# Optimization experiments

Measured on AMD Instinct MI355X. Metric: run time of the kernel, lower is better.

## Reference

```python
import jax, jax.numpy as jnp
import numpy as np
import math

B, N, H, D = 2, 2048, 16, 64

def setup_inputs() -> dict:
    key = jax.random.key(0)
    kq, kk, kv = jax.random.split(key, 3)
    q = jax.random.normal(kq, (B, N, H, D), dtype=jnp.float32)
    k = jax.random.normal(kk, (B, N, H, D), dtype=jnp.float32)
    v = jax.random.normal(kv, (B, N, H, D), dtype=jnp.float32)
    return {"q": q, "k": k, "v": v}

def reference(q, k, v):
    d = q.shape[-1]
    # [b,n,h,d] -> [b,h,n,d]
    qh = jnp.transpose(q, (0, 2, 1, 3))
    kh = jnp.transpose(k, (0, 2, 1, 3))
    vh = jnp.transpose(v, (0, 2, 1, 3))
    # scores: [b,h,n,n]
    scores = jnp.einsum('bhqd,bhkd->bhqk', qh, kh) / math.sqrt(d)
    # jax.nn.softmax performs the stable max-subtraction internally,
    # matching the original's explicit max-subtract + softmax.
    attn = jax.nn.softmax(scores, axis=-1)
    o = jnp.einsum('bhqk,bhkd->bhqd', attn, vh)
    # back to [b,n,h,d]
    return jnp.transpose(o, (0, 2, 1, 3))
```

## Files before the change

### kernel.cpp

```cpp
#include <hip/hip_runtime.h>


typedef float  f32x4  __attribute__((ext_vector_type(4)));
typedef float  f32x16 __attribute__((ext_vector_type(16)));
typedef short  s16x8  __attribute__((ext_vector_type(8)));
typedef short  s16x4  __attribute__((ext_vector_type(4)));
typedef int    i32x4  __attribute__((ext_vector_type(4)));

#define QSCALE 0.18033688011112042f

__device__ __forceinline__ unsigned short bf16r(float f) {
    unsigned u = __builtin_bit_cast(unsigned, f);
    u += 0x7fffu + ((u >> 16) & 1u);
    return (unsigned short)(u >> 16);
}

__device__ __forceinline__ s16x8 cvt8f_scaled(const float* p, float s) {
    f32x4 a = *(const f32x4*)p;
    f32x4 b = *(const f32x4*)(p + 4);
    s16x8 r;
#pragma unroll
    for (int i = 0; i < 4; ++i) {
        r[i]   = (short)bf16r(a[i] * s);
        r[i+4] = (short)bf16r(b[i] * s);
    }
    return r;
}

__device__ __forceinline__ int cvtpk2(float lo, float hi) {
    int r;
    asm("v_cvt_pk_bf16_f32 %0, %1, %2" : "=v"(r) : "v"(lo), "v"(hi));
    return r;
}

__global__ void __launch_bounds__(256)
prep(const float* __restrict__ K, const float* __restrict__ V,
     unsigned short* __restrict__ Kt, unsigned short* __restrict__ Vt) {
    const int t = threadIdx.x, bid = blockIdx.x;
    const int bh = bid & 31, nb = bid >> 5;
    const int b = bh >> 4, h = bh & 15;
    const size_t tile0 = ((size_t)bh * 64 + nb * 2) * 2048;

#pragma unroll
    for (int i = 0; i < 2; ++i) {
        const int lin = i * 256 + t;
        const int kbl = lin >> 8, rem = lin & 255;
        const int kc = rem >> 6, l = rem & 63;
        const int nl = l & 31, gg = l >> 5;
        const float* src = K + ((size_t)(b * 2048 + nb * 64 + kbl * 32 + nl)) * 1024
                             + h * 64 + kc * 16 + gg * 8;
        f32x4 a = *(const f32x4*)src;
        f32x4 c = *(const f32x4*)(src + 4);
        i32x4 o = { cvtpk2(a[0], a[1]), cvtpk2(a[2], a[3]),
                    cvtpk2(c[0], c[1]), cvtpk2(c[2], c[3]) };
        *(i32x4*)(Kt + tile0 + kbl * 2048 + kc * 512 + l * 8) = o;
    }

#pragma unroll
    for (int i = 0; i < 2; ++i) {
        const int lin = i * 256 + t;
        const int kbl = lin >> 8, rem = lin & 255;
        const int qq = rem >> 6, l = rem & 63;
        const int dt = qq >> 1, s = qq & 1;
        const int nl = l & 31, gg = l >> 5;
        const float* vp0 = V + ((size_t)(b * 2048 + nb * 64 + kbl * 32 + 8 * s + 4 * gg)) * 1024
                             + h * 64 + dt * 32 + nl;
        float x0 = vp0[0],     x1 = vp0[1024],  x2 = vp0[2048],  x3 = vp0[3072];
        float x4 = vp0[16384], x5 = vp0[17408], x6 = vp0[18432], x7 = vp0[19456];
        i32x4 o = { cvtpk2(x0, x1), cvtpk2(x2, x3),
                    cvtpk2(x4, x5), cvtpk2(x6, x7) };
        *(i32x4*)(Vt + tile0 + kbl * 2048 + qq * 512 + l * 8) = o;
    }
}

__global__ void __launch_bounds__(256, 2)
attn_fwd(const float* __restrict__ Q, const unsigned short* __restrict__ Kt,
         const unsigned short* __restrict__ Vt, float* __restrict__ O)
{
    __shared__ __align__(16) float ex[2 * 64 * 68];

    const int t = threadIdx.x;
    const int w = t >> 6, lane = t & 63;
    const int g = lane >> 5, nl = lane & 31;
    const int qsel = w & 1, ksel = w >> 1;

    const int bid = blockIdx.x;
    const int bh  = bid & 31, qb = bid >> 5;
    const int b   = bh >> 4,  h  = bh & 15;
    const int q0  = qb * 128 + qsel * 64;

    s16x8 qf[2][4];
#pragma unroll
    for (int qt = 0; qt < 2; ++qt) {
        const float* qp = Q + ((size_t)(b * 2048 + q0 + qt * 32 + nl)) * 1024
                            + h * 64 + g * 8;
#pragma unroll
        for (int kc = 0; kc < 4; ++kc)
            qf[qt][kc] = cvt8f_scaled(qp + kc * 16, QSCALE);
    }

    const unsigned short* kp = Kt + (size_t)bh * 131072 + (size_t)ksel * 65536 + lane * 8;
    const unsigned short* vp = Vt + (size_t)bh * 131072 + (size_t)ksel * 65536 + lane * 8;

    f32x16 oa00 = {}, oa01 = {}, oa10 = {}, oa11 = {};
    f32x16 sE, sO;
    f32x4  lpv0 = {}, lpv1 = {};

    s16x8 kf[4], vf[4];

#define QKCHAIN(DST, QFq) do {                                              \
        DST = (f32x16){};                                                   \
        __builtin_amdgcn_s_setprio(1);                                      \
        _Pragma("unroll")                                                   \
        for (int _kc = 0; _kc < 4; ++_kc)                                   \
            DST = __builtin_amdgcn_mfma_f32_32x32x16_bf16(                  \
                kf[_kc], QFq[_kc], DST, 0, 0, 0);                           \
        __builtin_amdgcn_s_setprio(0); } while (0)

#define EXPPK1(S, LPV, PK) do {                                             \
        _Pragma("unroll")                                                   \
        for (int _c = 0; _c < 4; ++_c) {                                    \
            f32x4 e = { __builtin_amdgcn_exp2f(S[4*_c]),                    \
                        __builtin_amdgcn_exp2f(S[4*_c+1]),                  \
                        __builtin_amdgcn_exp2f(S[4*_c+2]),                  \
                        __builtin_amdgcn_exp2f(S[4*_c+3]) };                \
            LPV += e;                                                       \
            PK[2*_c]   = cvtpk2(e[0], e[1]);                                \
            PK[2*_c+1] = cvtpk2(e[2], e[3]);                                \
        } } while (0)

#define PVQ(PK, OA0, OA1) do {                                              \
        __builtin_amdgcn_s_setprio(1);                                      \
        _Pragma("unroll")                                                   \
        for (int _s = 0; _s < 2; ++_s) {                                    \
            i32x4 bd = { PK[_s*2], PK[_s*2+1], PK[_s*2+4], PK[_s*2+5] };    \
            s16x8 bb = __builtin_bit_cast(s16x8, bd);                       \
            OA0 = __builtin_amdgcn_mfma_f32_32x32x16_bf16(vf[_s],     bb, OA0, 0, 0, 0); \
            OA1 = __builtin_amdgcn_mfma_f32_32x32x16_bf16(vf[2 + _s], bb, OA1, 0, 0, 0); \
        }                                                                   \
        __builtin_amdgcn_s_setprio(0); } while (0)

#define REFILL_K do {                                                       \
        _Pragma("unroll")                                                   \
        for (int _i = 0; _i < 4; ++_i)                                      \
            kf[_i] = *(const s16x8*)(kp + _i * 512); } while (0)
#define REFILL_V do {                                                       \
        _Pragma("unroll")                                                   \
        for (int _i = 0; _i < 4; ++_i)                                      \
            vf[_i] = *(const s16x8*)(vp + _i * 512); } while (0)

    REFILL_K;
    REFILL_V;
    kp += 2048;
    vp += 2048;
    QKCHAIN(sE, qf[0]);

#pragma unroll 1
    for (int m = 0; m < 31; ++m) {
        int pk[8];
        QKCHAIN(sO, qf[1]);
        REFILL_K;
        kp += 2048;
        EXPPK1(sE, lpv0, pk);
        PVQ(pk, oa00, oa10);
        QKCHAIN(sE, qf[0]);
        EXPPK1(sO, lpv1, pk);
        PVQ(pk, oa01, oa11);
        REFILL_V;
        vp += 2048;
    }
    {
        int pk[8];
        QKCHAIN(sO, qf[1]);
        EXPPK1(sE, lpv0, pk);
        PVQ(pk, oa00, oa10);
        EXPPK1(sO, lpv1, pk);
        PVQ(pk, oa01, oa11);
    }

#undef QKCHAIN
#undef EXPPK1
#undef PVQ
#undef REFILL_K
#undef REFILL_V

    float lp[2] = { lpv0[0] + lpv0[1] + lpv0[2] + lpv0[3],
                    lpv1[0] + lpv1[1] + lpv1[2] + lpv1[3] };

    __syncthreads();
    float* zone = ex + qsel * (64 * 68) + lane * 68;
    if (ksel) {
#pragma unroll
        for (int i = 0; i < 4; ++i) {
            *(f32x4*)(zone + i * 4) =
                (f32x4){ oa00[4*i], oa00[4*i+1], oa00[4*i+2], oa00[4*i+3] };
            *(f32x4*)(zone + 16 + i * 4) =
                (f32x4){ oa01[4*i], oa01[4*i+1], oa01[4*i+2], oa01[4*i+3] };
            *(f32x4*)(zone + 32 + i * 4) =
                (f32x4){ oa10[4*i], oa10[4*i+1], oa10[4*i+2], oa10[4*i+3] };
            *(f32x4*)(zone + 48 + i * 4) =
                (f32x4){ oa11[4*i], oa11[4*i+1], oa11[4*i+2], oa11[4*i+3] };
        }
        zone[64] = lp[0];
        zone[65] = lp[1];
    }
    __syncthreads();
    if (!ksel) {
#pragma unroll
        for (int i = 0; i < 4; ++i) {
            f32x4 u0 = *(const f32x4*)(zone + i * 4);
            f32x4 u1 = *(const f32x4*)(zone + 16 + i * 4);
            f32x4 u2 = *(const f32x4*)(zone + 32 + i * 4);
            f32x4 u3 = *(const f32x4*)(zone + 48 + i * 4);
#pragma unroll
            for (int j = 0; j < 4; ++j) {
                oa00[4*i+j] += u0[j]; oa01[4*i+j] += u1[j];
                oa10[4*i+j] += u2[j]; oa11[4*i+j] += u3[j];
            }
        }
        float inv[2];
#pragma unroll
        for (int qt = 0; qt < 2; ++qt) {
            float s = lp[qt] + zone[64 + qt];
            s += __shfl_xor(s, 32);
            inv[qt] = 1.0f / s;
        }
        float* op0 = O + ((size_t)(b * 2048 + q0 + nl)) * 1024 + h * 64;
        float* op1 = op0 + 32 * 1024;
#pragma unroll
        for (int rq = 0; rq < 4; ++rq) {
            const int d0 = 8 * rq + 4 * g;
            *(f32x4*)(op0 + d0) = (f32x4){
                oa00[4*rq]   * inv[0], oa00[4*rq+1] * inv[0],
                oa00[4*rq+2] * inv[0], oa00[4*rq+3] * inv[0] };
            *(f32x4*)(op0 + 32 + d0) = (f32x4){
                oa10[4*rq]   * inv[0], oa10[4*rq+1] * inv[0],
                oa10[4*rq+2] * inv[0], oa10[4*rq+3] * inv[0] };
            *(f32x4*)(op1 + d0) = (f32x4){
                oa01[4*rq]   * inv[1], oa01[4*rq+1] * inv[1],
                oa01[4*rq+2] * inv[1], oa01[4*rq+3] * inv[1] };
            *(f32x4*)(op1 + 32 + d0) = (f32x4){
                oa11[4*rq]   * inv[1], oa11[4*rq+1] * inv[1],
                oa11[4*rq+2] * inv[1], oa11[4*rq+3] * inv[1] };
        }
    }
}

extern "C" void kernel_launch(void* const* d_in, const int* in_sizes, int n_in,
                              void* d_out, int out_size, void* d_ws, size_t ws_size,
                              hipStream_t stream) {
    const float* q = (const float*)d_in[0];
    const float* k = (const float*)d_in[1];
    const float* v = (const float*)d_in[2];
    float* o = (float*)d_out;

    unsigned short* Kt = (unsigned short*)d_ws;
    unsigned short* Vt = Kt + 4194304;

    hipLaunchKernelGGL(prep,     dim3(1024), dim3(256), 0, stream, k, v, Kt, Vt);
    hipLaunchKernelGGL(attn_fwd, dim3(512),  dim3(256), 0, stream, q, Kt, Vt, o);
}
```

Baseline: 128.9 us.

## Ping-pong two wave groups per block with barrier-staggered QK and softmax-PV phases

Doubles the block to 512 threads covering 256 queries. The two halves of the block run offset schedules separated by s_barrier, so one group issues QK^T MFMAs while the other does exp/pack and PV MFMAs. The QK step now computes both query subtiles in one interleaved chain. This aims to overlap the exp (VALU) work with matrix-core work across waves and to hide load latency. The trade-offs are more barriers and a serialized two-pass reduction through shared memory at the end, and the grid shrinks to 256 blocks, which may leave some compute units underused.

```diff
diff --git a/kernel.cpp b/kernel.cpp
--- a/kernel.cpp
+++ b/kernel.cpp
@@ -73,7 +73,7 @@
     }
 }
 
-__global__ void __launch_bounds__(256, 2)
+__global__ void __launch_bounds__(512, 2)
 attn_fwd(const float* __restrict__ Q, const unsigned short* __restrict__ Kt,
          const unsigned short* __restrict__ Vt, float* __restrict__ O)
 {
@@ -82,12 +82,13 @@
     const int t = threadIdx.x;
     const int w = t >> 6, lane = t & 63;
     const int g = lane >> 5, nl = lane & 31;
-    const int qsel = w & 1, ksel = w >> 1;
+    const int phase = w >> 2;
+    const int qsel = w & 1, ksel = (w >> 1) & 1;
 
     const int bid = blockIdx.x;
     const int bh  = bid & 31, qb = bid >> 5;
     const int b   = bh >> 4,  h  = bh & 15;
-    const int q0  = qb * 128 + qsel * 64;
+    const int q0  = qb * 256 + phase * 128 + qsel * 64;
 
     s16x8 qf[2][4];
 #pragma unroll
@@ -103,145 +104,156 @@
     const unsigned short* vp = Vt + (size_t)bh * 131072 + (size_t)ksel * 65536 + lane * 8;
 
     f32x16 oa00 = {}, oa01 = {}, oa10 = {}, oa11 = {};
-    f32x16 sE, sO;
+    f32x16 sE0, sE1;
     f32x4  lpv0 = {}, lpv1 = {};
 
     s16x8 kf[4], vf[4];
 
-#define QKCHAIN(DST, QFq) do {                                              \
-        DST = (f32x16){};                                                   \
+#pragma unroll
+    for (int i = 0; i < 4; ++i) {
+        kf[i] = *(const s16x8*)(kp + i * 512);
+        vf[i] = *(const s16x8*)(vp + i * 512);
+    }
+    kp += 2048;
+    vp += 2048;
+
+#define REFILL_K do {                                                       \
+        _Pragma("unroll")                                                   \
+        for (int _i = 0; _i < 4; ++_i)                                      \
+            kf[_i] = *(const s16x8*)(kp + _i * 512);                        \
+        kp += 2048; } while (0)
+#define REFILL_V do {                                                       \
+        _Pragma("unroll")                                                   \
+        for (int _i = 0; _i < 4; ++_i)                                      \
+            vf[_i] = *(const s16x8*)(vp + _i * 512);                        \
+        vp += 2048; } while (0)
+
+#define QKT do {                                                            \
+        sE0 = (f32x16){}; sE1 = (f32x16){};                                 \
         __builtin_amdgcn_s_setprio(1);                                      \
         _Pragma("unroll")                                                   \
-        for (int _kc = 0; _kc < 4; ++_kc)                                   \
-            DST = __builtin_amdgcn_mfma_f32_32x32x16_bf16(                  \
-                kf[_kc], QFq[_kc], DST, 0, 0, 0);                           \
-        __builtin_amdgcn_s_setprio(0); } while (0)
-
-#define EXPPK1(S, LPV, PK) do {                                             \
-        _Pragma("unroll")                                                   \
-        for (int _c = 0; _c < 4; ++_c) {                                    \
-            f32x4 e = { __builtin_amdgcn_exp2f(S[4*_c]),                    \
-                        __builtin_amdgcn_exp2f(S[4*_c+1]),                  \
-                        __builtin_amdgcn_exp2f(S[4*_c+2]),                  \
-                        __builtin_amdgcn_exp2f(S[4*_c+3]) };                \
-            LPV += e;                                                       \
-            PK[2*_c]   = cvtpk2(e[0], e[1]);                                \
-            PK[2*_c+1] = cvtpk2(e[2], e[3]);                                \
-        } } while (0)
-
-#define PVQ(PK, OA0, OA1) do {                                              \
-        __builtin_amdgcn_s_setprio(1);                                      \
-        _Pragma("unroll")                                                   \
-        for (int _s = 0; _s < 2; ++_s) {                                    \
-            i32x4 bd = { PK[_s*2], PK[_s*2+1], PK[_s*2+4], PK[_s*2+5] };    \
-            s16x8 bb = __builtin_bit_cast(s16x8, bd);                       \
-            OA0 = __builtin_amdgcn_mfma_f32_32x32x16_bf16(vf[_s],     bb, OA0, 0, 0, 0); \
-            OA1 = __builtin_amdgcn_mfma_f32_32x32x16_bf16(vf[2 + _s], bb, OA1, 0, 0, 0); \
+        for (int _kc = 0; _kc < 4; ++_kc) {                                 \
+            sE0 = __builtin_amdgcn_mfma_f32_32x32x16_bf16(kf[_kc], qf[0][_kc], sE0, 0, 0, 0); \
+            sE1 = __builtin_amdgcn_mfma_f32_32x32x16_bf16(kf[_kc], qf[1][_kc], sE1, 0, 0, 0); \
         }                                                                   \
         __builtin_amdgcn_s_setprio(0); } while (0)
 
-#define REFILL_K do {                                                       \
-        _Pragma("unroll")                                                   \
-        for (int _i = 0; _i < 4; ++_i)                                      \
-            kf[_i] = *(const s16x8*)(kp + _i * 512); } while (0)
-#define REFILL_V do {                                                       \
-        _Pragma("unroll")                                                   \
-        for (int _i = 0; _i < 4; ++_i)                                      \
-            vf[_i] = *(const s16x8*)(vp + _i * 512); } while (0)
-
-    REFILL_K;
-    REFILL_V;
-    kp += 2048;
-    vp += 2048;
-    QKCHAIN(sE, qf[0]);
-
+#define SMPV do {                                                           \
+        int pk0[8], pk1[8];                                                 \
+        _Pragma("unroll")                                                   \
+        for (int _c = 0; _c < 4; ++_c) {                                    \
+            f32x4 e0 = { __builtin_amdgcn_exp2f(sE0[4*_c]),   __builtin_amdgcn_exp2f(sE0[4*_c+1]),  \
+                         __builtin_amdgcn_exp2f(sE0[4*_c+2]), __builtin_amdgcn_exp2f(sE0[4*_c+3]) };\
+            f32x4 e1 = { __builtin_amdgcn_exp2f(sE1[4*_c]),   __builtin_amdgcn_exp2f(sE1[4*_c+1]),  \
+                         __builtin_amdgcn_exp2f(sE1[4*_c+2]), __builtin_amdgcn_exp2f(sE1[4*_c+3]) };\
+            lpv0 += e0; lpv1 += e1;                                         \
+            pk0[2*_c]   = cvtpk2(e0[0], e0[1]);  pk0[2*_c+1] = cvtpk2(e0[2], e0[3]); \
+            pk1[2*_c]   = cvtpk2(e1[0], e1[1]);  pk1[2*_c+1] = cvtpk2(e1[2], e1[3]); \
+        }                                                                   \
+        __builtin_amdgcn_s_setprio(1);                                      \
+        _Pragma("unroll")                                                   \
+        for (int _s = 0; _s < 2; ++_s) {                                    \
+            i32x4 b0 = { pk0[_s*2], pk0[_s*2+1], pk0[_s*2+4], pk0[_s*2+5] };\
+            i32x4 b1 = { pk1[_s*2], pk1[_s*2+1], pk1[_s*2+4], pk1[_s*2+5] };\
+            s16x8 bb0 = __builtin_bit_cast(s16x8, b0);                      \
+            s16x8 bb1 = __builtin_bit_cast(s16x8, b1);                      \
+            oa00 = __builtin_amdgcn_mfma_f32_32x32x16_bf16(vf[_s],     bb0, oa00, 0, 0, 0); \
+            oa10 = __builtin_amdgcn_mfma_f32_32x32x16_bf16(vf[2 + _s], bb0, oa10, 0, 0, 0); \
+            oa01 = __builtin_amdgcn_mfma_f32_32x32x16_bf16(vf[_s],     bb1, oa01, 0, 0, 0); \
+            oa11 = __builtin_amdgcn_mfma_f32_32x32x16_bf16(vf[2 + _s], bb1, oa11, 0, 0, 0); \
+        }                                                                   \
+        __builtin_amdgcn_s_setprio(0); } while (0)
+
+    if (phase == 0) {
 #pragma unroll 1
-    for (int m = 0; m < 31; ++m) {
-        int pk[8];
-        QKCHAIN(sO, qf[1]);
+        for (int it = 0; it < 32; ++it) {
+            asm volatile("s_barrier");
+            QKT;
+            if (it < 31) REFILL_K;
+            SMPV;
+            if (it < 31) REFILL_V;
+        }
+    } else {
+        QKT;
         REFILL_K;
-        kp += 2048;
-        EXPPK1(sE, lpv0, pk);
-        PVQ(pk, oa00, oa10);
-        QKCHAIN(sE, qf[0]);
-        EXPPK1(sO, lpv1, pk);
-        PVQ(pk, oa01, oa11);
-        REFILL_V;
-        vp += 2048;
-    }
-    {
-        int pk[8];
-        QKCHAIN(sO, qf[1]);
-        EXPPK1(sE, lpv0, pk);
-        PVQ(pk, oa00, oa10);
-        EXPPK1(sO, lpv1, pk);
-        PVQ(pk, oa01, oa11);
-    }
-
-#undef QKCHAIN
-#undef EXPPK1
-#undef PVQ
+#pragma unroll 1
+        for (int it = 0; it < 32; ++it) {
+            asm volatile("s_barrier");
+            SMPV;
+            if (it < 31) REFILL_V;
+            if (it < 31) {
+                QKT;
+                if (it < 30) REFILL_K;
+            }
+        }
+    }
+
 #undef REFILL_K
 #undef REFILL_V
+#undef QKT
+#undef SMPV
 
     float lp[2] = { lpv0[0] + lpv0[1] + lpv0[2] + lpv0[3],
                     lpv1[0] + lpv1[1] + lpv1[2] + lpv1[3] };
 
-    __syncthreads();
     float* zone = ex + qsel * (64 * 68) + lane * 68;
-    if (ksel) {
-#pragma unroll
-        for (int i = 0; i < 4; ++i) {
-            *(f32x4*)(zone + i * 4) =
-                (f32x4){ oa00[4*i], oa00[4*i+1], oa00[4*i+2], oa00[4*i+3] };
-            *(f32x4*)(zone + 16 + i * 4) =
-                (f32x4){ oa01[4*i], oa01[4*i+1], oa01[4*i+2], oa01[4*i+3] };
-            *(f32x4*)(zone + 32 + i * 4) =
-                (f32x4){ oa10[4*i], oa10[4*i+1], oa10[4*i+2], oa10[4*i+3] };
-            *(f32x4*)(zone + 48 + i * 4) =
-                (f32x4){ oa11[4*i], oa11[4*i+1], oa11[4*i+2], oa11[4*i+3] };
-        }
-        zone[64] = lp[0];
-        zone[65] = lp[1];
-    }
-    __syncthreads();
-    if (!ksel) {
-#pragma unroll
-        for (int i = 0; i < 4; ++i) {
-            f32x4 u0 = *(const f32x4*)(zone + i * 4);
-            f32x4 u1 = *(const f32x4*)(zone + 16 + i * 4);
-            f32x4 u2 = *(const f32x4*)(zone + 32 + i * 4);
-            f32x4 u3 = *(const f32x4*)(zone + 48 + i * 4);
-#pragma unroll
-            for (int j = 0; j < 4; ++j) {
-                oa00[4*i+j] += u0[j]; oa01[4*i+j] += u1[j];
-                oa10[4*i+j] += u2[j]; oa11[4*i+j] += u3[j];
-            }
-        }
-        float inv[2];
-#pragma unroll
-        for (int qt = 0; qt < 2; ++qt) {
-            float s = lp[qt] + zone[64 + qt];
-            s += __shfl_xor(s, 32);
-            inv[qt] = 1.0f / s;
-        }
-        float* op0 = O + ((size_t)(b * 2048 + q0 + nl)) * 1024 + h * 64;
-        float* op1 = op0 + 32 * 1024;
-#pragma unroll
-        for (int rq = 0; rq < 4; ++rq) {
-            const int d0 = 8 * rq + 4 * g;
-            *(f32x4*)(op0 + d0) = (f32x4){
-                oa00[4*rq]   * inv[0], oa00[4*rq+1] * inv[0],
-                oa00[4*rq+2] * inv[0], oa00[4*rq+3] * inv[0] };
-            *(f32x4*)(op0 + 32 + d0) = (f32x4){
-                oa10[4*rq]   * inv[0], oa10[4*rq+1] * inv[0],
-                oa10[4*rq+2] * inv[0], oa10[4*rq+3] * inv[0] };
-            *(f32x4*)(op1 + d0) = (f32x4){
-                oa01[4*rq]   * inv[1], oa01[4*rq+1] * inv[1],
-                oa01[4*rq+2] * inv[1], oa01[4*rq+3] * inv[1] };
-            *(f32x4*)(op1 + 32 + d0) = (f32x4){
-                oa11[4*rq]   * inv[1], oa11[4*rq+1] * inv[1],
-                oa11[4*rq+2] * inv[1], oa11[4*rq+3] * inv[1] };
+#pragma unroll 1
+    for (int p = 0; p < 2; ++p) {
+        __syncthreads();
+        if (phase == p && ksel) {
+#pragma unroll
+            for (int i = 0; i < 4; ++i) {
+                *(f32x4*)(zone + i * 4) =
+                    (f32x4){ oa00[4*i], oa00[4*i+1], oa00[4*i+2], oa00[4*i+3] };
+                *(f32x4*)(zone + 16 + i * 4) =
+                    (f32x4){ oa01[4*i], oa01[4*i+1], oa01[4*i+2], oa01[4*i+3] };
+                *(f32x4*)(zone + 32 + i * 4) =
+                    (f32x4){ oa10[4*i], oa10[4*i+1], oa10[4*i+2], oa10[4*i+3] };
+                *(f32x4*)(zone + 48 + i * 4) =
+                    (f32x4){ oa11[4*i], oa11[4*i+1], oa11[4*i+2], oa11[4*i+3] };
+            }
+            zone[64] = lp[0];
+            zone[65] = lp[1];
+        }
+        __syncthreads();
+        if (phase == p && !ksel) {
+#pragma unroll
+            for (int i = 0; i < 4; ++i) {
+                f32x4 u0 = *(const f32x4*)(zone + i * 4);
+                f32x4 u1 = *(const f32x4*)(zone + 16 + i * 4);
+                f32x4 u2 = *(const f32x4*)(zone + 32 + i * 4);
+                f32x4 u3 = *(const f32x4*)(zone + 48 + i * 4);
+#pragma unroll
+                for (int j = 0; j < 4; ++j) {
+                    oa00[4*i+j] += u0[j]; oa01[4*i+j] += u1[j];
+                    oa10[4*i+j] += u2[j]; oa11[4*i+j] += u3[j];
+                }
+            }
+            float inv[2];
+#pragma unroll
+            for (int qt = 0; qt < 2; ++qt) {
+                float s = lp[qt] + zone[64 + qt];
+                s += __shfl_xor(s, 32);
+                inv[qt] = 1.0f / s;
+            }
+            float* op0 = O + ((size_t)(b * 2048 + q0 + nl)) * 1024 + h * 64;
+            float* op1 = op0 + 32 * 1024;
+#pragma unroll
+            for (int rq = 0; rq < 4; ++rq) {
+                const int d0 = 8 * rq + 4 * g;
+                *(f32x4*)(op0 + d0) = (f32x4){
+                    oa00[4*rq]   * inv[0], oa00[4*rq+1] * inv[0],
+                    oa00[4*rq+2] * inv[0], oa00[4*rq+3] * inv[0] };
+                *(f32x4*)(op0 + 32 + d0) = (f32x4){
+                    oa10[4*rq]   * inv[0], oa10[4*rq+1] * inv[0],
+                    oa10[4*rq+2] * inv[0], oa10[4*rq+3] * inv[0] };
+                *(f32x4*)(op1 + d0) = (f32x4){
+                    oa01[4*rq]   * inv[1], oa01[4*rq+1] * inv[1],
+                    oa01[4*rq+2] * inv[1], oa01[4*rq+3] * inv[1] };
+                *(f32x4*)(op1 + 32 + d0) = (f32x4){
+                    oa11[4*rq]   * inv[1], oa11[4*rq+1] * inv[1],
+                    oa11[4*rq+2] * inv[1], oa11[4*rq+3] * inv[1] };
+            }
         }
     }
 }
@@ -258,5 +270,5 @@
     unsigned short* Vt = Kt + 4194304;
 
     hipLaunchKernelGGL(prep,     dim3(1024), dim3(256), 0, stream, k, v, Kt, Vt);
-    hipLaunchKernelGGL(attn_fwd, dim3(512),  dim3(256), 0, stream, q, Kt, Vt, o);
-}
+    hipLaunchKernelGGL(attn_fwd, dim3(256),  dim3(512), 0, stream, q, Kt, Vt, o);
+}
```

After: 130.7 us. No clear change (+1.4%).
